# Kernel optimization log

Hardware: AMD Instinct MI355X
Metric: run time of the kernel (lower is better)

Reference implementation:

```python
import jax, jax.numpy as jnp
import numpy as np
from jax import lax

TOTAL_LENGTH = 1024
EMBED_DIM = 128
GRAPH_DIM = 50257
N_STEP = 128  # min_len
BATCH = 32


def setup_inputs() -> dict:
    key = jax.random.key(0)
    k1, k2, k3, k4, k5, k6, k7 = jax.random.split(key, 7)
    s_e = 1.0 / np.sqrt(EMBED_DIM)
    return {
        "zi": jax.random.randint(k1, (BATCH,), 0, TOTAL_LENGTH),
        "y": jax.random.randint(k2, (BATCH, N_STEP), 0, GRAPH_DIM),
        "latent": jax.random.normal(k3, (TOTAL_LENGTH, EMBED_DIM), dtype=jnp.float32) * s_e,
        "Wt": jax.random.normal(k4, (EMBED_DIM, EMBED_DIM), dtype=jnp.float32) * s_e,
        "bt": jax.random.normal(k5, (EMBED_DIM,), dtype=jnp.float32) * s_e,
        "Wv": jax.random.normal(k6, (GRAPH_DIM, EMBED_DIM), dtype=jnp.float32) * s_e,
        "bv": jax.random.normal(k7, (GRAPH_DIM,), dtype=jnp.float32) * s_e,
    }


def reference(zi, y, latent, Wt, bt, Wv, bv):
    # z0: [B, E] gathered from latent table
    z0 = latent[zi]

    def step(z, _):
        # emit current z, then update: z <- tanh(z + transition(z))
        z_next = jnp.tanh(z + z @ Wt.T + bt)
        return z_next, z

    _, zs = lax.scan(step, z0, None, length=N_STEP)  # [T, B, E]
    zs = jnp.transpose(zs, (1, 0, 2))                # [B, T, E]
    logits = jnp.einsum("bte,ve->btv", zs, Wv) + bv  # [B, T, V]
    ys = jax.nn.log_softmax(logits, axis=-1)
    yp = jnp.take_along_axis(ys, y[:, :, None], axis=-1)[:, :, 0]  # [B, T]
    return yp
```

## Files before the change

### kernel.cpp

```cpp
#include <hip/hip_runtime.h>
#include <hip/hip_bf16.h>
#include <hip/hip_fp8.h>

#define EMBED 128
#define TSTEPS 128
#define NBATCH 32
#define VDIM 50257
#define VPAD 50304
#define MROWS 4096
#define NGROUPS 786
#define GRIDX 64
#define GRIDY 32
#define MAXGRP 13
#define CONV_N4 ((VDIM * EMBED) / 4)
#define CONV_BLOCKS ((CONV_N4 + 255) / 256)

static constexpr float LOG2E = 1.4426950408889634f;
static constexpr float LN2   = 0.6931471805599453f;

__device__ __forceinline__ float fast_exp2(float x) {
#if __has_builtin(__builtin_amdgcn_exp2f)
    return __builtin_amdgcn_exp2f(x);
#else
    return exp2f(x);
#endif
}
__device__ __forceinline__ float fast_log2(float x) {
#if __has_builtin(__builtin_amdgcn_logf)
    return __builtin_amdgcn_logf(x);
#else
    return log2f(x);
#endif
}
__device__ __forceinline__ float fast_rcp(float x) {
#if __has_builtin(__builtin_amdgcn_rcpf)
    return __builtin_amdgcn_rcpf(x);
#else
    return 1.0f / x;
#endif
}
__device__ __forceinline__ float fast_tanh_nr(float x) {
    x = fminf(20.0f, fmaxf(-20.0f, x));
    float t = fast_exp2((2.0f * LOG2E) * x);
    float u = t + 1.0f;
    float r = fast_rcp(u);
    r = r * fmaf(-u, r, 2.0f);
    return (t - 1.0f) * r;
}
__device__ __forceinline__ unsigned short f2bf_raw(float f) {
    __hip_bfloat16 h = __float2bfloat16(f);
    union { __hip_bfloat16 b; unsigned short u; } cvt;
    cvt.b = h;
    return cvt.u;
}
__device__ __forceinline__ float bf_raw2f(unsigned short u) {
    union { unsigned int u; float f; } cvt;
    cvt.u = ((unsigned int)u) << 16;
    return cvt.f;
}
template <bool HI>
__device__ __forceinline__ int pk_fp8(float a, float b, int old) {
#if __has_builtin(__builtin_amdgcn_cvt_pk_fp8_f32)
    return __builtin_amdgcn_cvt_pk_fp8_f32(a, b, old, HI);
#else
    __hip_fp8_e4m3 x(a), y(b);
    int v = (int)(unsigned char)x.__x | ((int)(unsigned char)y.__x << 8);
    return HI ? ((old & 0xffff) | (v << 16)) : ((old & ~0xffff) | v);
#endif
}

__global__ __launch_bounds__(256) void setup_kernel(const int* __restrict__ zi,
                                                    const float* __restrict__ latent,
                                                    const float* __restrict__ Wt,
                                                    const float* __restrict__ bt,
                                                    const float* __restrict__ Wv,
                                                    const float* __restrict__ bv,
                                                    unsigned short* __restrict__ zsb,
                                                    unsigned char* __restrict__ zsa8,
                                                    unsigned char* __restrict__ wv8,
                                                    float* __restrict__ bvs,
                                                    float* __restrict__ S) {
    if (blockIdx.x >= NBATCH) {
        const int cb = blockIdx.x - NBATCH;
        if (cb == 0) {
#pragma unroll
            for (int i = 0; i < MROWS / 256; i++)
                S[i * 256 + threadIdx.x] = 0.f;
        }
        if (cb == 1) {
            const int base  = VDIM * EMBED / 4;
            const int npad  = (VPAD - VDIM) * EMBED / 4;
            for (int i = threadIdx.x; i < npad; i += 256)
                reinterpret_cast<unsigned int*>(wv8)[base + i] = 0u;
        }
        const int idx = cb * 256 + threadIdx.x;
        if (idx < VPAD)
            bvs[idx] = (idx < VDIM) ? bv[idx] * LOG2E : -1e30f;
        if (idx < CONV_N4) {
            float4 v = reinterpret_cast<const float4*>(Wv)[idx];
            int p = pk_fp8<false>(v.x, v.y, 0);
            p = pk_fp8<true>(v.z, v.w, p);
            reinterpret_cast<unsigned int*>(wv8)[idx] = (unsigned int)p;
        }
        return;
    }

    __shared__ float zbuf[2][EMBED];
    __shared__ unsigned short zstash[TSTEPS * EMBED];
    const int b = blockIdx.x;
    const int e = threadIdx.x >> 1;
    const int h = threadIdx.x & 1;

    float4 wrow[16];
    const float4* wt4 = reinterpret_cast<const float4*>(Wt + e * EMBED + h * 64);
#pragma unroll
    for (int i = 0; i < 16; i++) wrow[i] = wt4[i];
    const float bte = bt[e];

    if (h == 0) zbuf[0][e] = latent[zi[b] * EMBED + e];
    __syncthreads();

    int cur = 0;
    for (int t = 0; t < TSTEPS; t++) {
        const float zc = zbuf[cur][e];
        if (h == 0)
            zstash[t * EMBED + e] = f2bf_raw(zc * LOG2E);

        const float4* z4 = reinterpret_cast<const float4*>(&zbuf[cur][h * 64]);
        float4 acc = {0.f, 0.f, 0.f, 0.f};
#pragma unroll
        for (int i = 0; i < 16; i++) {
            float4 zv = z4[i];
            acc.x += zv.x * wrow[i].x;
            acc.y += zv.y * wrow[i].y;
            acc.z += zv.z * wrow[i].z;
            acc.w += zv.w * wrow[i].w;
        }
        float v = acc.x + acc.y + acc.z + acc.w;
        float p = __shfl_xor(v, 1);
        float sA = h ? p : v;
        float sB = h ? v : p;
        float znew = fast_tanh_nr(((zc + sA) + sB) + bte);
        if (h == 0) zbuf[cur ^ 1][e] = znew;
        __syncthreads();
        cur ^= 1;
    }

    uint4* dstb = reinterpret_cast<uint4*>(zsb + (long)b * TSTEPS * EMBED);
    uint2* dsta = reinterpret_cast<uint2*>(zsa8 + (long)b * TSTEPS * EMBED);
    const uint4* src = reinterpret_cast<const uint4*>(zstash);
    for (int i = threadIdx.x; i < TSTEPS * EMBED / 8; i += 256) {
        uint4 w = src[i];
        dstb[i] = w;
        float f0 = bf_raw2f(w.x & 0xffff), f1 = bf_raw2f(w.x >> 16);
        float f2 = bf_raw2f(w.y & 0xffff), f3 = bf_raw2f(w.y >> 16);
        float f4 = bf_raw2f(w.z & 0xffff), f5 = bf_raw2f(w.z >> 16);
        float f6 = bf_raw2f(w.w & 0xffff), f7 = bf_raw2f(w.w >> 16);
        int lo = pk_fp8<false>(f0, f1, 0); lo = pk_fp8<true>(f2, f3, lo);
        int hi = pk_fp8<false>(f4, f5, 0); hi = pk_fp8<true>(f6, f7, hi);
        uint2 o; o.x = (unsigned int)lo; o.y = (unsigned int)hi;
        dsta[i] = o;
    }
}

typedef __attribute__((ext_vector_type(4))) float f32x4;

__global__ __launch_bounds__(256) void gemm_lse_kernel(const unsigned char* __restrict__ zsa8,
                                                       const unsigned char* __restrict__ wv8,
                                                       const float* __restrict__ bvs,
                                                       float* __restrict__ S) {
    __shared__ unsigned char ldsb[2][8192];
    __shared__ float ldsbias[MAXGRP * 64];

    const int lane  = threadIdx.x & 63;
    const int wave  = threadIdx.x >> 6;
    const int col16 = lane & 15;
    const int quad  = lane >> 4;
    const int mbase = blockIdx.y * 128 + wave * 32;

    const int x  = blockIdx.x;
    const int g0 = x * 12 + min(x, 18);
    const int g1 = g0 + 12 + (x < 18 ? 1 : 0);
    const int nbias = (g1 - g0) * 64;

    for (int i = threadIdx.x; i < nbias; i += 256)
        ldsbias[i] = bvs[g0 * 64 + i];

    unsigned long long a[2][4];
#pragma unroll
    for (int s = 0; s < 2; s++)
#pragma unroll
        for (int c = 0; c < 4; c++)
            a[s][c] = *reinterpret_cast<const unsigned long long*>(
                zsa8 + (long)(mbase + s * 16 + col16) * EMBED + c * 32 + quad * 8);

    float sums[8];
#pragma unroll
    for (int i = 0; i < 8; i++) sums[i] = 0.f;

    auto stage = [&](int buf, int g) {
#pragma unroll
        for (int j = 0; j < 2; j++) {
            const int rr = (wave * 2 + j) * 8 + (lane >> 3);
            const int G  = (lane & 7) ^ (rr & 7);
            const unsigned char* gp = wv8 + (long)(g * 64 + rr) * EMBED + G * 16;
            __builtin_amdgcn_global_load_lds(
                (const __attribute__((address_space(1))) void*)gp,
                (__attribute__((address_space(3))) void*)&ldsb[buf][(wave * 2 + j) * 1024],
                16, 0, 0);
        }
    };

    int cur = 0;
    stage(0, g0);

    const f32x4 dzero = {0.f, 0.f, 0.f, 0.f};

    for (int g = g0; g < g1; g++) {
        __syncthreads();
        if (g + 1 < g1) stage(cur ^ 1, g + 1);

        const float* biasg = &ldsbias[(g - g0) * 64];

#pragma unroll
        for (int c = 0; c < 4; c++) {
            const unsigned char* rowp = &ldsb[cur][(c * 16 + col16) * 128];
            const int r7 = col16 & 7;
            unsigned long long bf[4];
#pragma unroll
            for (int kc = 0; kc < 4; kc++) {
                const int q_abs = kc * 4 + quad;
                bf[kc] = *reinterpret_cast<const unsigned long long*>(
                    rowp + (((q_abs >> 1) ^ r7) * 16) + ((q_abs & 1) * 8));
            }

            const float eb = fast_exp2(biasg[c * 16 + col16]);

            f32x4 d[2];
#pragma unroll
            for (int s = 0; s < 2; s++)
                d[s] = __builtin_amdgcn_mfma_f32_16x16x32_fp8_fp8(
                    (long long)a[s][0], (long long)bf[0], dzero, 0, 0, 0);
#pragma unroll
            for (int kc = 1; kc < 4; kc++)
#pragma unroll
                for (int s = 0; s < 2; s++)
                    d[s] = __builtin_amdgcn_mfma_f32_16x16x32_fp8_fp8(
                        (long long)a[s][kc], (long long)bf[kc], d[s], 0, 0, 0);

#pragma unroll
            for (int s = 0; s < 2; s++)
#pragma unroll
                for (int r = 0; r < 4; r++)
                    sums[s * 4 + r] = fmaf(fast_exp2(d[s][r]), eb, sums[s * 4 + r]);
        }
        cur ^= 1;
    }

#pragma unroll
    for (int s = 0; s < 2; s++) {
#pragma unroll
        for (int r = 0; r < 4; r++) {
            float v = sums[s * 4 + r];
            v += __shfl_xor(v, 1);
            v += __shfl_xor(v, 2);
            v += __shfl_xor(v, 4);
            v += __shfl_xor(v, 8);
            if (col16 == 0)
                atomicAdd(&S[mbase + s * 16 + quad * 4 + r], v);
        }
    }
}

__global__ __launch_bounds__(256) void tail_kernel(const unsigned short* __restrict__ zsb,
                                                   const float* __restrict__ Wv,
                                                   const float* __restrict__ bv,
                                                   const int* __restrict__ y,
                                                   const float* __restrict__ S,
                                                   float* __restrict__ out) {
    const int row  = blockIdx.x * 4 + (threadIdx.x >> 6);
    const int lane = threadIdx.x & 63;
    const int yv = y[row];
    const ushort2* zr = reinterpret_cast<const ushort2*>(zsb + (long)row * EMBED);
    const float2*  wr = reinterpret_cast<const float2*>(Wv + (long)yv * EMBED);
    ushort2 z2 = zr[lane];
    float2  w2 = wr[lane];
    float v = bf_raw2f(z2.x) * w2.x + bf_raw2f(z2.y) * w2.y;
    v += __shfl_xor(v, 32);
    v += __shfl_xor(v, 16);
    v += __shfl_xor(v, 8);
    v += __shfl_xor(v, 4);
    v += __shfl_xor(v, 2);
    v += __shfl_xor(v, 1);
    if (lane == 0)
        out[row] = LN2 * (v - fast_log2(S[row])) + bv[yv];
}

extern "C" void kernel_launch(void* const* d_in, const int* in_sizes, int n_in,
                              void* d_out, int out_size, void* d_ws, size_t ws_size,
                              hipStream_t stream) {
    const int*   zi     = (const int*)d_in[0];
    const int*   y      = (const int*)d_in[1];
    const float* latent = (const float*)d_in[2];
    const float* Wt     = (const float*)d_in[3];
    const float* bt     = (const float*)d_in[4];
    const float* Wv     = (const float*)d_in[5];
    const float* bv     = (const float*)d_in[6];
    float* out = (float*)d_out;

    char* ws = (char*)d_ws;
    unsigned short* zsb  = (unsigned short*)ws;
    unsigned char*  zsa8 = (unsigned char*)(ws + (1u << 20));
    float*          S    = (float*)(ws + 1536u * 1024);
    float*          bvs  = (float*)(ws + 1536u * 1024 + (64u << 10));
    unsigned char*  wv8  = (unsigned char*)(ws + (2u << 20));

    setup_kernel<<<NBATCH + CONV_BLOCKS, 256, 0, stream>>>(zi, latent, Wt, bt, Wv, bv,
                                                           zsb, zsa8, wv8, bvs, S);

    gemm_lse_kernel<<<dim3(GRIDX, GRIDY), 256, 0, stream>>>(zsa8, wv8, bvs, S);

    tail_kernel<<<MROWS / 4, 256, 0, stream>>>(zsb, Wv, bv, y, S, out);
}
```

Baseline: 195.6 us.

## Fuse tail kernel into GEMM-LSE via last-block-done counter per row group

Removes the separate tail kernel launch. Each GEMM block increments a per-blockIdx.y counter after its atomic adds to S, and the last block to finish for a row group computes the target-logit dot products and writes the final log-probabilities. This saves one kernel launch and its gap, at the cost of a fence plus atomic per block and a serialized tail of 128 rows done by a single block at the end.

```diff
diff --git a/kernel.cpp b/kernel.cpp
--- a/kernel.cpp
+++ b/kernel.cpp
@@ -79,13 +79,16 @@
                                                     unsigned char* __restrict__ zsa8,
                                                     unsigned char* __restrict__ wv8,
                                                     float* __restrict__ bvs,
-                                                    float* __restrict__ S) {
+                                                    float* __restrict__ S,
+                                                    int* __restrict__ cnt) {
     if (blockIdx.x >= NBATCH) {
         const int cb = blockIdx.x - NBATCH;
         if (cb == 0) {
 #pragma unroll
             for (int i = 0; i < MROWS / 256; i++)
                 S[i * 256 + threadIdx.x] = 0.f;
+            if (threadIdx.x < GRIDY)
+                cnt[threadIdx.x] = 0;
         }
         if (cb == 1) {
             const int base  = VDIM * EMBED / 4;
@@ -168,9 +171,16 @@
 __global__ __launch_bounds__(256) void gemm_lse_kernel(const unsigned char* __restrict__ zsa8,
                                                        const unsigned char* __restrict__ wv8,
                                                        const float* __restrict__ bvs,
-                                                       float* __restrict__ S) {
+                                                       float* __restrict__ S,
+                                                       const unsigned short* __restrict__ zsb,
+                                                       const float* __restrict__ Wv,
+                                                       const float* __restrict__ bv,
+                                                       const int* __restrict__ yidx,
+                                                       float* __restrict__ out,
+                                                       int* __restrict__ cnt) {
     __shared__ unsigned char ldsb[2][8192];
     __shared__ float ldsbias[MAXGRP * 64];
+    __shared__ int lastflag;
 
     const int lane  = threadIdx.x & 63;
     const int wave  = threadIdx.x >> 6;
@@ -270,30 +280,36 @@
                 atomicAdd(&S[mbase + s * 16 + quad * 4 + r], v);
         }
     }
-}
-
-__global__ __launch_bounds__(256) void tail_kernel(const unsigned short* __restrict__ zsb,
-                                                   const float* __restrict__ Wv,
-                                                   const float* __restrict__ bv,
-                                                   const int* __restrict__ y,
-                                                   const float* __restrict__ S,
-                                                   float* __restrict__ out) {
-    const int row  = blockIdx.x * 4 + (threadIdx.x >> 6);
-    const int lane = threadIdx.x & 63;
-    const int yv = y[row];
-    const ushort2* zr = reinterpret_cast<const ushort2*>(zsb + (long)row * EMBED);
-    const float2*  wr = reinterpret_cast<const float2*>(Wv + (long)yv * EMBED);
-    ushort2 z2 = zr[lane];
-    float2  w2 = wr[lane];
-    float v = bf_raw2f(z2.x) * w2.x + bf_raw2f(z2.y) * w2.y;
-    v += __shfl_xor(v, 32);
-    v += __shfl_xor(v, 16);
-    v += __shfl_xor(v, 8);
-    v += __shfl_xor(v, 4);
-    v += __shfl_xor(v, 2);
-    v += __shfl_xor(v, 1);
-    if (lane == 0)
-        out[row] = LN2 * (v - fast_log2(S[row])) + bv[yv];
+
+    __syncthreads();
+    if (threadIdx.x == 0) {
+        __threadfence();
+        int old = __hip_atomic_fetch_add(&cnt[blockIdx.y], 1,
+                                         __ATOMIC_ACQ_REL, __HIP_MEMORY_SCOPE_AGENT);
+        lastflag = (old == GRIDX - 1);
+    }
+    __syncthreads();
+    if (lastflag) {
+#pragma unroll 2
+        for (int i = 0; i < 32; i++) {
+            const int row = blockIdx.y * 128 + wave * 32 + i;
+            const int yv  = yidx[row];
+            ushort2 z2 = reinterpret_cast<const ushort2*>(zsb + (long)row * EMBED)[lane];
+            float2  w2 = reinterpret_cast<const float2*>(Wv + (long)yv * EMBED)[lane];
+            float v = bf_raw2f(z2.x) * w2.x + bf_raw2f(z2.y) * w2.y;
+            v += __shfl_xor(v, 32);
+            v += __shfl_xor(v, 16);
+            v += __shfl_xor(v, 8);
+            v += __shfl_xor(v, 4);
+            v += __shfl_xor(v, 2);
+            v += __shfl_xor(v, 1);
+            if (lane == 0) {
+                float Sv = __hip_atomic_load(&S[row], __ATOMIC_RELAXED,
+                                             __HIP_MEMORY_SCOPE_AGENT);
+                out[row] = LN2 * (v - fast_log2(Sv)) + bv[yv];
+            }
+        }
+    }
 }
 
 extern "C" void kernel_launch(void* const* d_in, const int* in_sizes, int n_in,
@@ -312,13 +328,13 @@
     unsigned short* zsb  = (unsigned short*)ws;
     unsigned char*  zsa8 = (unsigned char*)(ws + (1u << 20));
     float*          S    = (float*)(ws + 1536u * 1024);
+    int*            cnt  = (int*)(ws + 1536u * 1024 + (16u << 10));
     float*          bvs  = (float*)(ws + 1536u * 1024 + (64u << 10));
     unsigned char*  wv8  = (unsigned char*)(ws + (2u << 20));
 
     setup_kernel<<<NBATCH + CONV_BLOCKS, 256, 0, stream>>>(zi, latent, Wt, bt, Wv, bv,
-                                                           zsb, zsa8, wv8, bvs, S);
-
-    gemm_lse_kernel<<<dim3(GRIDX, GRIDY), 256, 0, stream>>>(zsa8, wv8, bvs, S);
-
-    tail_kernel<<<MROWS / 4, 256, 0, stream>>>(zsb, Wv, bv, y, S, out);
-}
+                                                           zsb, zsa8, wv8, bvs, S, cnt);
+
+    gemm_lse_kernel<<<dim3(GRIDX, GRIDY), 256, 0, stream>>>(zsa8, wv8, bvs, S,
+                                                            zsb, Wv, bv, y, out, cnt);
+}
```

Result: slower. 281.7 us (+44.0%).

## Split vocab columns across waves and keep all 128 rows of A in registers

Applied to the files above, without the earlier changes.

Each wave now owns 16 vocab columns of every 64-column group and holds all 128 fp8 activation rows in registers, instead of splitting rows across waves and sharing the Wv tile through double-buffered LDS. B fragments and biases are loaded straight from global memory into registers with a one-group prefetch, which removes the LDS staging, bias preload and per-group __syncthreads. The cost is much higher register pressure (32 A values and 32 accumulators per lane), plus global loads that are less coalesced and no longer overlapped through LDS.

```diff
diff --git a/kernel.cpp b/kernel.cpp
--- a/kernel.cpp
+++ b/kernel.cpp
@@ -11,7 +11,6 @@
 #define NGROUPS 786
 #define GRIDX 64
 #define GRIDY 32
-#define MAXGRP 13
 #define CONV_N4 ((VDIM * EMBED) / 4)
 #define CONV_BLOCKS ((CONV_N4 + 255) / 256)
 
@@ -169,96 +168,81 @@
                                                        const unsigned char* __restrict__ wv8,
                                                        const float* __restrict__ bvs,
                                                        float* __restrict__ S) {
-    __shared__ unsigned char ldsb[2][8192];
-    __shared__ float ldsbias[MAXGRP * 64];
-
     const int lane  = threadIdx.x & 63;
     const int wave  = threadIdx.x >> 6;
     const int col16 = lane & 15;
     const int quad  = lane >> 4;
-    const int mbase = blockIdx.y * 128 + wave * 32;
+    const int mbase = blockIdx.y * 128;
 
     const int x  = blockIdx.x;
     const int g0 = x * 12 + min(x, 18);
     const int g1 = g0 + 12 + (x < 18 ? 1 : 0);
-    const int nbias = (g1 - g0) * 64;
-
-    for (int i = threadIdx.x; i < nbias; i += 256)
-        ldsbias[i] = bvs[g0 * 64 + i];
-
-    unsigned long long a[2][4];
-#pragma unroll
-    for (int s = 0; s < 2; s++)
-#pragma unroll
-        for (int c = 0; c < 4; c++)
-            a[s][c] = *reinterpret_cast<const unsigned long long*>(
-                zsa8 + (long)(mbase + s * 16 + col16) * EMBED + c * 32 + quad * 8);
-
-    float sums[8];
-#pragma unroll
-    for (int i = 0; i < 8; i++) sums[i] = 0.f;
-
-    auto stage = [&](int buf, int g) {
-#pragma unroll
-        for (int j = 0; j < 2; j++) {
-            const int rr = (wave * 2 + j) * 8 + (lane >> 3);
-            const int G  = (lane & 7) ^ (rr & 7);
-            const unsigned char* gp = wv8 + (long)(g * 64 + rr) * EMBED + G * 16;
-            __builtin_amdgcn_global_load_lds(
-                (const __attribute__((address_space(1))) void*)gp,
-                (__attribute__((address_space(3))) void*)&ldsb[buf][(wave * 2 + j) * 1024],
-                16, 0, 0);
-        }
-    };
-
-    int cur = 0;
-    stage(0, g0);
+
+    unsigned long long a[8][4];
+#pragma unroll
+    for (int s = 0; s < 8; s++)
+#pragma unroll
+        for (int kc = 0; kc < 4; kc++)
+            a[s][kc] = *reinterpret_cast<const unsigned long long*>(
+                zsa8 + (long)(mbase + s * 16 + col16) * EMBED + kc * 32 + quad * 8);
+
+    float sums[32];
+#pragma unroll
+    for (int i = 0; i < 32; i++) sums[i] = 0.f;
+
+    const unsigned char* bp = wv8 + (long)(g0 * 64 + wave * 16 + col16) * EMBED + quad * 8;
+    const float* bvp = bvs + g0 * 64 + wave * 16 + col16;
+
+    unsigned long long bfc[4];
+#pragma unroll
+    for (int kc = 0; kc < 4; kc++)
+        bfc[kc] = *reinterpret_cast<const unsigned long long*>(bp + kc * 32);
+    float ebc = *bvp;
 
     const f32x4 dzero = {0.f, 0.f, 0.f, 0.f};
 
     for (int g = g0; g < g1; g++) {
-        __syncthreads();
-        if (g + 1 < g1) stage(cur ^ 1, g + 1);
-
-        const float* biasg = &ldsbias[(g - g0) * 64];
-
-#pragma unroll
-        for (int c = 0; c < 4; c++) {
-            const unsigned char* rowp = &ldsb[cur][(c * 16 + col16) * 128];
-            const int r7 = col16 & 7;
-            unsigned long long bf[4];
-#pragma unroll
-            for (int kc = 0; kc < 4; kc++) {
-                const int q_abs = kc * 4 + quad;
-                bf[kc] = *reinterpret_cast<const unsigned long long*>(
-                    rowp + (((q_abs >> 1) ^ r7) * 16) + ((q_abs & 1) * 8));
-            }
-
-            const float eb = fast_exp2(biasg[c * 16 + col16]);
-
-            f32x4 d[2];
-#pragma unroll
-            for (int s = 0; s < 2; s++)
-                d[s] = __builtin_amdgcn_mfma_f32_16x16x32_fp8_fp8(
-                    (long long)a[s][0], (long long)bf[0], dzero, 0, 0, 0);
+        unsigned long long bf[4];
+#pragma unroll
+        for (int kc = 0; kc < 4; kc++) bf[kc] = bfc[kc];
+        const float ebv = ebc;
+
+        if (g + 1 < g1) {
+            bp  += 64 * EMBED;
+            bvp += 64;
+#pragma unroll
+            for (int kc = 0; kc < 4; kc++)
+                bfc[kc] = *reinterpret_cast<const unsigned long long*>(bp + kc * 32);
+            ebc = *bvp;
+        }
+
+        const float eb = fast_exp2(ebv);
+
+#pragma unroll
+        for (int half = 0; half < 2; half++) {
+            f32x4 d[4];
+#pragma unroll
+            for (int ss = 0; ss < 4; ss++)
+                d[ss] = __builtin_amdgcn_mfma_f32_16x16x32_fp8_fp8(
+                    (long long)a[half * 4 + ss][0], (long long)bf[0], dzero, 0, 0, 0);
 #pragma unroll
             for (int kc = 1; kc < 4; kc++)
 #pragma unroll
-                for (int s = 0; s < 2; s++)
-                    d[s] = __builtin_amdgcn_mfma_f32_16x16x32_fp8_fp8(
-                        (long long)a[s][kc], (long long)bf[kc], d[s], 0, 0, 0);
-
-#pragma unroll
-            for (int s = 0; s < 2; s++)
+                for (int ss = 0; ss < 4; ss++)
+                    d[ss] = __builtin_amdgcn_mfma_f32_16x16x32_fp8_fp8(
+                        (long long)a[half * 4 + ss][kc], (long long)bf[kc], d[ss], 0, 0, 0);
+
+#pragma unroll
+            for (int ss = 0; ss < 4; ss++)
 #pragma unroll
                 for (int r = 0; r < 4; r++)
-                    sums[s * 4 + r] = fmaf(fast_exp2(d[s][r]), eb, sums[s * 4 + r]);
-        }
-        cur ^= 1;
-    }
-
-#pragma unroll
-    for (int s = 0; s < 2; s++) {
+                    sums[(half * 4 + ss) * 4 + r] =
+                        fmaf(fast_exp2(d[ss][r]), eb, sums[(half * 4 + ss) * 4 + r]);
+        }
+    }
+
+#pragma unroll
+    for (int s = 0; s < 8; s++) {
 #pragma unroll
         for (int r = 0; r < 4; r++) {
             float v = sums[s * 4 + r];
```

After: 279.3 us. +42.8%, slower.
